# Kernel optimization log

Measured on AMD Instinct MI355X. Metric: run time of the kernel, lower is better.

## Reference

```python
import jax, jax.numpy as jnp
import numpy as np

KERNEL_NUM = 21
SIGMA = 0.1
EXACT_SIGMA = 0.001
EPS = 1e-8  # torch F.cosine_similarity eps


def _kernel_params():
    n = KERNEL_NUM - 1
    mus = [1.0 / n + 2.0 * i / n - 1.0 for i in range(n)] + [1.0]
    sigmas = [SIGMA] * n + [EXACT_SIGMA]
    return jnp.asarray(mus, jnp.float32), jnp.asarray(sigmas, jnp.float32)


def setup_inputs() -> dict:
    key = jax.random.key(0)
    ks = jax.random.split(key, 12)
    B, QL, DL, V, D = 512, 32, 256, 100000, 256
    return {
        "query_1": jax.random.randint(ks[0], (B, QL), 0, V),
        "document_1": jax.random.randint(ks[1], (B, DL), 0, V),
        "query_2": jax.random.randint(ks[2], (B, QL), 0, V),
        "document_2": jax.random.randint(ks[3], (B, DL), 0, V),
        "emb_weight": jax.random.normal(ks[4], (V, D), jnp.float32),
        "W0": jax.random.normal(ks[5], (10, 21), jnp.float32) * 0.2,
        "b0": jax.random.normal(ks[6], (10,), jnp.float32) * 0.1,
        "W1": jax.random.normal(ks[7], (5, 10), jnp.float32) * 0.3,
        "b1": jax.random.normal(ks[8], (5,), jnp.float32) * 0.1,
        "W2": jax.random.normal(ks[9], (1, 5), jnp.float32) * 0.4,
        "b2": jax.random.normal(ks[10], (1,), jnp.float32) * 0.1,
    }


def _predict(query, doc, emb_weight, W0, b0, W1, b1, W2, b2):
    q = emb_weight[query]  # [B, QL, D]
    d = emb_weight[doc]    # [B, DL, D]
    qn = q / jnp.maximum(jnp.linalg.norm(q, axis=-1, keepdims=True), EPS)
    dn = d / jnp.maximum(jnp.linalg.norm(d, axis=-1, keepdims=True), EPS)
    mm = jnp.einsum('bqe,bde->bqd', qn, dn)  # cosine matching matrix [B,QL,DL]
    mus, sigmas = _kernel_params()
    # Gaussian soft binning: [B,QL,DL,K]
    K = jnp.exp(-0.5 * (mm[..., None] - mus) ** 2 / sigmas ** 2)
    km = jnp.log1p(K.sum(axis=2)).sum(axis=1)  # [B, K]
    h = jax.nn.relu(km @ W0.T + b0)
    h = jax.nn.relu(h @ W1.T + b1)
    return h @ W2.T + b2  # [B, 1]


def reference(query_1, document_1, query_2, document_2,
              emb_weight, W0, b0, W1, b1, W2, b2):
    l1 = _predict(query_1, document_1, emb_weight, W0, b0, W1, b1, W2, b2)
    l2 = _predict(query_2, document_2, emb_weight, W0, b0, W1, b1, W2, b2)
    return jax.nn.sigmoid(l1 - l2)
```

## Files before the change

kernel.cpp:

```cpp
#include <hip/hip_runtime.h>
#include <math.h>

typedef __bf16 bf16x8 __attribute__((ext_vector_type(8)));
typedef __bf16 bf16x4 __attribute__((ext_vector_type(4)));
typedef float  f32x4  __attribute__((ext_vector_type(4)));

#define QL    32
#define DL    256
#define DIM   256
#define NK    21
#define KSOFT 20
#define STR   264
#define L2E   1.4426950408889634f

#if __has_builtin(__builtin_amdgcn_exp2f)
#define EXP2F(x) __builtin_amdgcn_exp2f(x)
#else
#define EXP2F(x) exp2f(x)
#endif

#define EVAL_BINS(mm, ACC0)                                                  \
    {                                                                        \
        float U  = EXP2F(L2E * fmaf(10.0f, (mm), 9.0f));                     \
        float t0 = (mm) + 0.95f;                                             \
        float E  = EXP2F((-50.0f * L2E) * t0 * t0);                          \
        ACC0[0] += E;                                                        \
        E *= U;                           ACC0[1]  += E;          \
        E *= U * 0.36787944117144233f;    ACC0[2]  += E;          \
        E *= U * 0.1353352832366127f;     ACC0[3]  += E;          \
        E *= U * 0.049787068367863944f;   ACC0[4]  += E;          \
        E *= U * 0.018315638888734179f;   ACC0[5]  += E;          \
        E *= U * 0.006737946999085467f;   ACC0[6]  += E;          \
        float t7 = (mm) + 0.25f;                                             \
        E = EXP2F((-50.0f * L2E) * t7 * t7);                                 \
        ACC0[7] += E;                                                        \
        E *= U * 0.0009118819655545162f;  ACC0[8]  += E;          \
        E *= U * 0.00033546262790251185f; ACC0[9]  += E;          \
        E *= U * 0.0001234098040866796f;  ACC0[10] += E;          \
        E *= U * 4.5399929762484854e-05f; ACC0[11] += E;          \
        E *= U * 1.670170079024566e-05f;  ACC0[12] += E;          \
        E *= U * 6.14421235332821e-06f;   ACC0[13] += E;          \
        float t14 = (mm) - 0.45f;                                            \
        E = EXP2F((-50.0f * L2E) * t14 * t14);                               \
        ACC0[14] += E;                                                       \
        E *= U * 8.315287191035679e-07f;  ACC0[15] += E;          \
        E *= U * 3.059023205018258e-07f;  ACC0[16] += E;          \
        E *= U * 1.1253517471925912e-07f; ACC0[17] += E;          \
        E *= U * 4.139937718785167e-08f;  ACC0[18] += E;          \
        E *= U * 1.522997974471263e-08f;  ACC0[19] += E;          \
    }

__global__ __launch_bounds__(256)
void knrm_prep(const float* __restrict__ emb, __bf16* __restrict__ tab, int V)
{
    const int wave = threadIdx.x >> 6;
    const int lane = threadIdx.x & 63;
    const int row0 = (blockIdx.x * 4 + wave) * 2;
    if (row0 >= V) return;

    float4 a = reinterpret_cast<const float4*>(emb + (size_t)row0 * DIM)[lane];
    float4 c = reinterpret_cast<const float4*>(emb + (size_t)(row0 + 1) * DIM)[lane];
    float sa = a.x*a.x + a.y*a.y + a.z*a.z + a.w*a.w;
    float sc = c.x*c.x + c.y*c.y + c.z*c.z + c.w*c.w;
    #pragma unroll
    for (int m = 32; m; m >>= 1) { sa += __shfl_xor(sa, m); sc += __shfl_xor(sc, m); }
    float ia = rsqrtf(fmaxf(sa, 1e-16f));
    float ic = rsqrtf(fmaxf(sc, 1e-16f));
    bf16x4 oa, oc;
    oa[0] = (__bf16)(a.x * ia); oa[1] = (__bf16)(a.y * ia);
    oa[2] = (__bf16)(a.z * ia); oa[3] = (__bf16)(a.w * ia);
    oc[0] = (__bf16)(c.x * ic); oc[1] = (__bf16)(c.y * ic);
    oc[2] = (__bf16)(c.z * ic); oc[3] = (__bf16)(c.w * ic);
    *reinterpret_cast<bf16x4*>(tab + (size_t)row0 * DIM + lane * 4) = oa;
    *reinterpret_cast<bf16x4*>(tab + (size_t)(row0 + 1) * DIM + lane * 4) = oc;
}

__global__ __launch_bounds__(256, 4)
void knrm_main8(const int* __restrict__ q1t, const int* __restrict__ d1t,
                const int* __restrict__ q2t, const int* __restrict__ d2t,
                const __bf16* __restrict__ tab,
                const float* __restrict__ W0, const float* __restrict__ b0,
                const float* __restrict__ W1, const float* __restrict__ b1,
                const float* __restrict__ W2, const float* __restrict__ b2,
                float* __restrict__ lg, int B)
{
    const int b    = blockIdx.x;
    const int pair = blockIdx.y;
    const int tid  = threadIdx.x;
    const int wave = tid >> 6;
    const int lane = tid & 63;
    const int qt   = wave >> 1;
    const int dt   = wave & 1;
    const int g    = lane >> 4;
    const int cl   = lane & 15;
    const int hl   = lane & 31;
    const int hw   = lane >> 5;

    const int* qtok = pair ? q2t : q1t;
    const int* dtok = pair ? d2t : d1t;

    __shared__ __align__(16) __bf16 qbuf[QL * STR];
    __shared__ __align__(16) __bf16 dbuf[32 * STR];
    __shared__ float Sqk[QL * NK];
    __shared__ int   dtok_s[DL];
    __shared__ int   qtok_s[QL];
    __shared__ float km[NK];
    __shared__ float h0[10];
    __shared__ float h1[5];

    if (tid < QL) qtok_s[tid] = qtok[b * QL + tid];
    dtok_s[tid] = dtok[b * DL + tid];
    for (int e = tid; e < QL * NK; e += 256) Sqk[e] = 0.0f;
    if (tid < NK) km[tid] = 0.0f;
    __syncthreads();

    {
        bf16x8 qv[4];
        #pragma unroll
        for (int i = 0; i < 4; ++i) {
            int r = wave * 8 + i * 2 + hw;
            qv[i] = *reinterpret_cast<const bf16x8*>(
                tab + (size_t)qtok_s[r] * DIM + hl * 8);
        }
        #pragma unroll
        for (int i = 0; i < 4; ++i) {
            int r = wave * 8 + i * 2 + hw;
            *reinterpret_cast<bf16x8*>(&qbuf[r * STR + hl * 8]) = qv[i];
        }
    }

    bf16x8 dreg[4];
    #pragma unroll
    for (int i = 0; i < 4; ++i) {
        int r = wave * 8 + i * 2 + hw;
        dreg[i] = *reinterpret_cast<const bf16x8*>(
            tab + (size_t)dtok_s[r] * DIM + hl * 8);
    }

    const int myq  = qt * 16 + cl;
    const int qtk1 = qtok_s[myq];

    float acc[NK];
    #pragma unroll
    for (int k = 0; k < NK; ++k) acc[k] = 0.0f;

    for (int tile = 0; tile < 8; ++tile) {
        __syncthreads();

        #pragma unroll
        for (int i = 0; i < 4; ++i) {
            int r = wave * 8 + i * 2 + hw;
            *reinterpret_cast<bf16x8*>(&dbuf[r * STR + hl * 8]) = dreg[i];
        }
        if (tile < 7) {
            #pragma unroll
            for (int i = 0; i < 4; ++i) {
                int r = wave * 8 + i * 2 + hw;
                dreg[i] = *reinterpret_cast<const bf16x8*>(
                    tab + (size_t)dtok_s[(tile + 1) * 32 + r] * DIM + hl * 8);
            }
        }
        __syncthreads();

        f32x4 cf = {0.0f, 0.0f, 0.0f, 0.0f};
        #pragma unroll
        for (int ks = 0; ks < 8; ++ks) {
            bf16x8 dfr = *reinterpret_cast<const bf16x8*>(&dbuf[(dt*16 + cl)*STR + ks*32 + g*8]);
            bf16x8 qfr = *reinterpret_cast<const bf16x8*>(&qbuf[(qt*16 + cl)*STR + ks*32 + g*8]);
            cf = __builtin_amdgcn_mfma_f32_16x16x32_bf16(dfr, qfr, cf, 0, 0, 0);
        }

        #pragma unroll
        for (int i = 0; i < 4; ++i) {
            float mm = cf[i];
            EVAL_BINS(mm, acc);
            int drow = tile*32 + dt*16 + g*4 + i;
            acc[KSOFT] += (dtok_s[drow] == qtk1) ? 1.0f : 0.0f;
        }
    }

    #pragma unroll
    for (int k = 0; k < NK; ++k)
        atomicAdd(&Sqk[myq * NK + k], acc[k]);
    __syncthreads();

    for (int e = tid; e < QL * NK; e += 256)
        atomicAdd(&km[e % NK], log1pf(Sqk[e]));
    __syncthreads();

    if (tid < 10) {
        float h = b0[tid];
        #pragma unroll
        for (int k = 0; k < NK; ++k) h = fmaf(km[k], W0[tid*NK + k], h);
        h0[tid] = fmaxf(h, 0.0f);
    }
    __syncthreads();
    if (tid < 5) {
        float h = b1[tid];
        #pragma unroll
        for (int j = 0; j < 10; ++j) h = fmaf(h0[j], W1[tid*10 + j], h);
        h1[tid] = fmaxf(h, 0.0f);
    }
    __syncthreads();
    if (tid == 0) {
        float l = b2[0];
        #pragma unroll
        for (int j = 0; j < 5; ++j) l = fmaf(h1[j], W2[j], l);
        lg[pair * B + b] = l;
    }
}

__global__ void knrm_final(const float* __restrict__ lg, float* __restrict__ out, int B)
{
    int i = blockIdx.x * 256 + threadIdx.x;
    if (i < B) {
        float z = lg[i] - lg[B + i];
        out[i] = 1.0f / (1.0f + expf(-z));
    }
}

__global__ __launch_bounds__(256, 2)
void knrm_mono(const int* __restrict__ q1t, const int* __restrict__ d1t,
               const int* __restrict__ q2t, const int* __restrict__ d2t,
               const float* __restrict__ emb,
               const float* __restrict__ W0, const float* __restrict__ b0,
               const float* __restrict__ W1, const float* __restrict__ b1,
               const float* __restrict__ W2, const float* __restrict__ b2,
               float* __restrict__ out)
{
    const int b    = blockIdx.x;
    const int tid  = threadIdx.x;
    const int wave = tid >> 6;
    const int lane = tid & 63;
    const int qt   = wave >> 1;
    const int dt   = wave & 1;
    const int g    = lane >> 4;
    const int cl   = lane & 15;

    __shared__ __align__(16) __bf16 qbuf[QL * STR];
    __shared__ __align__(16) __bf16 dbuf[32 * STR];
    __shared__ float Sqk[QL * NK];
    __shared__ int   dtok_s[DL];
    __shared__ int   qtok_s[QL];
    __shared__ float km[NK];
    __shared__ float h0[10];
    __shared__ float h1[5];
    __shared__ float logit[2];

    for (int pair = 0; pair < 2; ++pair) {
        const int* qtok = pair ? q2t : q1t;
        const int* dtok = pair ? d2t : d1t;

        if (tid < QL) qtok_s[tid] = qtok[b * QL + tid];
        dtok_s[tid] = dtok[b * DL + tid];
        for (int e = tid; e < QL * NK; e += 256) Sqk[e] = 0.0f;
        if (tid < NK) km[tid] = 0.0f;
        __syncthreads();

        #pragma unroll
        for (int i = 0; i < 8; ++i) {
            int row = wave * 8 + i;
            int tok = qtok_s[row];
            float4 v = reinterpret_cast<const float4*>(emb + (size_t)tok * DIM)[lane];
            float s = v.x*v.x + v.y*v.y + v.z*v.z + v.w*v.w;
            #pragma unroll
            for (int m = 32; m; m >>= 1) s += __shfl_xor(s, m);
            float inv = rsqrtf(fmaxf(s, 1e-16f));
            bf16x4 o;
            o[0] = (__bf16)(v.x * inv); o[1] = (__bf16)(v.y * inv);
            o[2] = (__bf16)(v.z * inv); o[3] = (__bf16)(v.w * inv);
            *reinterpret_cast<bf16x4*>(&qbuf[row * STR + lane * 4]) = o;
        }

        int qtk[4];
        #pragma unroll
        for (int i = 0; i < 4; ++i) qtk[i] = qtok_s[qt * 16 + g * 4 + i];

        float acc[4 * NK];
        #pragma unroll
        for (int e = 0; e < 4 * NK; ++e) acc[e] = 0.0f;

        for (int tile = 0; tile < 8; ++tile) {
            #pragma unroll
            for (int i = 0; i < 8; ++i) {
                int r = wave * 8 + i;
                int tok = dtok_s[tile * 32 + r];
                float4 v = reinterpret_cast<const float4*>(emb + (size_t)tok * DIM)[lane];
                float s = v.x*v.x + v.y*v.y + v.z*v.z + v.w*v.w;
                #pragma unroll
                for (int m = 32; m; m >>= 1) s += __shfl_xor(s, m);
                float inv = rsqrtf(fmaxf(s, 1e-16f));
                bf16x4 o;
                o[0] = (__bf16)(v.x * inv); o[1] = (__bf16)(v.y * inv);
                o[2] = (__bf16)(v.z * inv); o[3] = (__bf16)(v.w * inv);
                *reinterpret_cast<bf16x4*>(&dbuf[r * STR + lane * 4]) = o;
            }
            __syncthreads();

            f32x4 cf = {0.0f, 0.0f, 0.0f, 0.0f};
            #pragma unroll
            for (int ks = 0; ks < 8; ++ks) {
                bf16x8 af  = *reinterpret_cast<const bf16x8*>(&qbuf[(qt*16 + cl)*STR + ks*32 + g*8]);
                bf16x8 bfr = *reinterpret_cast<const bf16x8*>(&dbuf[(dt*16 + cl)*STR + ks*32 + g*8]);
                cf = __builtin_amdgcn_mfma_f32_16x16x32_bf16(af, bfr, cf, 0, 0, 0);
            }

            int dtk = dtok_s[tile*32 + dt*16 + cl];
            #pragma unroll
            for (int i = 0; i < 4; ++i) {
                float mm = cf[i];
                float* a4 = &acc[i*NK];
                EVAL_BINS(mm, a4);
                a4[KSOFT] += (dtk == qtk[i]) ? 1.0f : 0.0f;
            }
            __syncthreads();
        }

        #pragma unroll
        for (int i = 0; i < 4; ++i) {
            int row = qt*16 + g*4 + i;
            #pragma unroll
            for (int k = 0; k < NK; ++k)
                atomicAdd(&Sqk[row*NK + k], acc[i*NK + k]);
        }
        __syncthreads();

        for (int e = tid; e < QL * NK; e += 256)
            atomicAdd(&km[e % NK], log1pf(Sqk[e]));
        __syncthreads();

        if (tid < 10) {
            float h = b0[tid];
            #pragma unroll
            for (int k = 0; k < NK; ++k) h = fmaf(km[k], W0[tid*NK + k], h);
            h0[tid] = fmaxf(h, 0.0f);
        }
        __syncthreads();
        if (tid < 5) {
            float h = b1[tid];
            #pragma unroll
            for (int j = 0; j < 10; ++j) h = fmaf(h0[j], W1[tid*10 + j], h);
            h1[tid] = fmaxf(h, 0.0f);
        }
        __syncthreads();
        if (tid == 0) {
            float l = b2[0];
            #pragma unroll
            for (int j = 0; j < 5; ++j) l = fmaf(h1[j], W2[j], l);
            logit[pair] = l;
        }
        __syncthreads();
    }

    if (tid == 0) {
        float z = logit[0] - logit[1];
        out[b] = 1.0f / (1.0f + expf(-z));
    }
}

extern "C" void kernel_launch(void* const* d_in, const int* in_sizes, int n_in,
                              void* d_out, int out_size, void* d_ws, size_t ws_size,
                              hipStream_t stream) {
    const int*   q1  = (const int*)d_in[0];
    const int*   d1  = (const int*)d_in[1];
    const int*   q2  = (const int*)d_in[2];
    const int*   d2  = (const int*)d_in[3];
    const float* emb = (const float*)d_in[4];
    const float* W0  = (const float*)d_in[5];
    const float* b0  = (const float*)d_in[6];
    const float* W1  = (const float*)d_in[7];
    const float* b1  = (const float*)d_in[8];
    const float* W2  = (const float*)d_in[9];
    const float* b2  = (const float*)d_in[10];
    float* out = (float*)d_out;

    const int B = in_sizes[0] / QL;
    const int V = in_sizes[4] / DIM;

    size_t tab_bytes = (size_t)V * DIM * sizeof(__bf16);
    size_t need = tab_bytes + 256 + (size_t)2 * B * sizeof(float);

    if (ws_size >= need) {
        __bf16* tab = (__bf16*)d_ws;
        float*  lg  = (float*)((char*)d_ws + ((tab_bytes + 255) & ~(size_t)255));

        knrm_prep<<<(V/2 + 3) / 4, 256, 0, stream>>>(emb, tab, V);
        dim3 grid(B, 2);
        knrm_main8<<<grid, 256, 0, stream>>>(q1, d1, q2, d2, tab,
                                             W0, b0, W1, b1, W2, b2, lg, B);
        knrm_final<<<(B + 255) / 256, 256, 0, stream>>>(lg, out, B);
    } else {
        knrm_mono<<<B, 256, 0, stream>>>(q1, d1, q2, d2, emb,
                                         W0, b0, W1, b1, W2, b2, out);
    }
}
```

Baseline: 235.9 us.

## Use 32x32 MFMA with document rows loaded directly into registers

Replaces the tiled 16x16x32 MFMA loop, which staged document embeddings through shared memory with double-buffered registers and per-tile barriers, with 32x32x16 MFMA. Each wave now handles 64 document rows and loads its A-operand fragments straight from the global bf16 table. Only the query matrix stays in LDS. This removes the dbuf LDS traffic and 16 barriers, at the cost of exposing the global gather latency without software prefetch and holding more accumulators and fragment registers.

```diff
diff --git a/kernel.cpp b/kernel.cpp
--- a/kernel.cpp
+++ b/kernel.cpp
@@ -4,6 +4,7 @@
 typedef __bf16 bf16x8 __attribute__((ext_vector_type(8)));
 typedef __bf16 bf16x4 __attribute__((ext_vector_type(4)));
 typedef float  f32x4  __attribute__((ext_vector_type(4)));
+typedef float  f32x16 __attribute__((ext_vector_type(16)));
 
 #define QL    32
 #define DL    256
@@ -76,7 +77,7 @@
 }
 
 __global__ __launch_bounds__(256, 4)
-void knrm_main8(const int* __restrict__ q1t, const int* __restrict__ d1t,
+void knrm_main9(const int* __restrict__ q1t, const int* __restrict__ d1t,
                 const int* __restrict__ q2t, const int* __restrict__ d2t,
                 const __bf16* __restrict__ tab,
                 const float* __restrict__ W0, const float* __restrict__ b0,
@@ -89,18 +90,13 @@
     const int tid  = threadIdx.x;
     const int wave = tid >> 6;
     const int lane = tid & 63;
-    const int qt   = wave >> 1;
-    const int dt   = wave & 1;
-    const int g    = lane >> 4;
-    const int cl   = lane & 15;
-    const int hl   = lane & 31;
+    const int l31  = lane & 31;
     const int hw   = lane >> 5;
 
     const int* qtok = pair ? q2t : q1t;
     const int* dtok = pair ? d2t : d1t;
 
     __shared__ __align__(16) __bf16 qbuf[QL * STR];
-    __shared__ __align__(16) __bf16 dbuf[32 * STR];
     __shared__ float Sqk[QL * NK];
     __shared__ int   dtok_s[DL];
     __shared__ int   qtok_s[QL];
@@ -112,76 +108,72 @@
     dtok_s[tid] = dtok[b * DL + tid];
     for (int e = tid; e < QL * NK; e += 256) Sqk[e] = 0.0f;
     if (tid < NK) km[tid] = 0.0f;
-    __syncthreads();
-
+
+    __syncthreads();
     {
         bf16x8 qv[4];
         #pragma unroll
         for (int i = 0; i < 4; ++i) {
             int r = wave * 8 + i * 2 + hw;
             qv[i] = *reinterpret_cast<const bf16x8*>(
-                tab + (size_t)qtok_s[r] * DIM + hl * 8);
+                tab + (size_t)qtok_s[r] * DIM + l31 * 8);
         }
         #pragma unroll
         for (int i = 0; i < 4; ++i) {
             int r = wave * 8 + i * 2 + hw;
-            *reinterpret_cast<bf16x8*>(&qbuf[r * STR + hl * 8]) = qv[i];
-        }
-    }
-
-    bf16x8 dreg[4];
-    #pragma unroll
-    for (int i = 0; i < 4; ++i) {
-        int r = wave * 8 + i * 2 + hw;
-        dreg[i] = *reinterpret_cast<const bf16x8*>(
-            tab + (size_t)dtok_s[r] * DIM + hl * 8);
-    }
-
-    const int myq  = qt * 16 + cl;
-    const int qtk1 = qtok_s[myq];
+            *reinterpret_cast<bf16x8*>(&qbuf[r * STR + l31 * 8]) = qv[i];
+        }
+    }
+    __syncthreads();
+
+    const int qtk1 = qtok_s[l31];
 
     float acc[NK];
     #pragma unroll
     for (int k = 0; k < NK; ++k) acc[k] = 0.0f;
 
-    for (int tile = 0; tile < 8; ++tile) {
-        __syncthreads();
-
-        #pragma unroll
-        for (int i = 0; i < 4; ++i) {
-            int r = wave * 8 + i * 2 + hw;
-            *reinterpret_cast<bf16x8*>(&dbuf[r * STR + hl * 8]) = dreg[i];
-        }
-        if (tile < 7) {
-            #pragma unroll
-            for (int i = 0; i < 4; ++i) {
-                int r = wave * 8 + i * 2 + hw;
-                dreg[i] = *reinterpret_cast<const bf16x8*>(
-                    tab + (size_t)dtok_s[(tile + 1) * 32 + r] * DIM + hl * 8);
-            }
-        }
-        __syncthreads();
-
-        f32x4 cf = {0.0f, 0.0f, 0.0f, 0.0f};
+    #pragma unroll
+    for (int t = 0; t < 2; ++t) {
+        const int dbase = wave * 64 + t * 32;
+        const int tokA  = dtok_s[dbase + l31];
+        const __bf16* abase = tab + (size_t)tokA * DIM + hw * 8;
+
+        f32x16 mc;
+        #pragma unroll
+        for (int j = 0; j < 16; ++j) mc[j] = 0.0f;
+
+        bf16x8 af[8];
+        #pragma unroll
+        for (int ks = 0; ks < 8; ++ks)
+            af[ks] = *reinterpret_cast<const bf16x8*>(abase + ks * 16);
         #pragma unroll
         for (int ks = 0; ks < 8; ++ks) {
-            bf16x8 dfr = *reinterpret_cast<const bf16x8*>(&dbuf[(dt*16 + cl)*STR + ks*32 + g*8]);
-            bf16x8 qfr = *reinterpret_cast<const bf16x8*>(&qbuf[(qt*16 + cl)*STR + ks*32 + g*8]);
-            cf = __builtin_amdgcn_mfma_f32_16x16x32_bf16(dfr, qfr, cf, 0, 0, 0);
-        }
-
-        #pragma unroll
-        for (int i = 0; i < 4; ++i) {
-            float mm = cf[i];
+            bf16x8 bf = *reinterpret_cast<const bf16x8*>(
+                &qbuf[l31 * STR + ks * 16 + hw * 8]);
+            mc = __builtin_amdgcn_mfma_f32_32x32x16_bf16(af[ks], bf, mc, 0, 0, 0);
+        }
+        #pragma unroll
+        for (int ks = 0; ks < 8; ++ks)
+            af[ks] = *reinterpret_cast<const bf16x8*>(abase + 128 + ks * 16);
+        #pragma unroll
+        for (int ks = 0; ks < 8; ++ks) {
+            bf16x8 bf = *reinterpret_cast<const bf16x8*>(
+                &qbuf[l31 * STR + 128 + ks * 16 + hw * 8]);
+            mc = __builtin_amdgcn_mfma_f32_32x32x16_bf16(af[ks], bf, mc, 0, 0, 0);
+        }
+
+        #pragma unroll
+        for (int r = 0; r < 16; ++r) {
+            float mm = mc[r];
             EVAL_BINS(mm, acc);
-            int drow = tile*32 + dt*16 + g*4 + i;
-            acc[KSOFT] += (dtok_s[drow] == qtk1) ? 1.0f : 0.0f;
+            int crow = dbase + (r & 3) + 8 * (r >> 2) + 4 * hw;
+            acc[KSOFT] += (dtok_s[crow] == qtk1) ? 1.0f : 0.0f;
         }
     }
 
     #pragma unroll
     for (int k = 0; k < NK; ++k)
-        atomicAdd(&Sqk[myq * NK + k], acc[k]);
+        atomicAdd(&Sqk[l31 * NK + k], acc[k]);
     __syncthreads();
 
     for (int e = tid; e < QL * NK; e += 256)
@@ -386,7 +378,7 @@
 
         knrm_prep<<<(V/2 + 3) / 4, 256, 0, stream>>>(emb, tab, V);
         dim3 grid(B, 2);
-        knrm_main8<<<grid, 256, 0, stream>>>(q1, d1, q2, d2, tab,
+        knrm_main9<<<grid, 256, 0, stream>>>(q1, d1, q2, d2, tab,
                                              W0, b0, W1, b1, W2, b2, lg, B);
         knrm_final<<<(B + 255) / 256, 256, 0, stream>>>(lg, out, B);
     } else {
```

Measured after the change: 237.5 us. About the same (+0.7%).
